# Performance work log

Hardware: AMD Instinct MI355X
Metric: run time of the kernel (lower is better)

The kernel has to match this reference:

```python
import jax, jax.numpy as jnp
import numpy as np

EMBED_DIM = 1024
NUM_HEADS = 16
NUM_GROUPS = 4
HEAD_DIM = EMBED_DIM // NUM_HEADS
REPEAT = NUM_HEADS // NUM_GROUPS
MAX_TIME = 128
MAX_FREQ = 8


def build_relative_index(q_len, k_len, freq_size=MAX_FREQ, max_time=MAX_TIME, max_freq=MAX_FREQ):
    # static (numpy) construction; shapes are compile-time constants under jit
    q_time = q_len // max_freq
    k_time = k_len // max_freq
    qt = np.arange(q_time) + (k_time - q_time)
    q_coords = np.stack(np.meshgrid(qt, np.arange(freq_size), indexing='ij')).reshape(2, -1)
    k_coords = np.stack(np.meshgrid(np.arange(k_time), np.arange(freq_size), indexing='ij')).reshape(2, -1)
    rel = q_coords[:, :, None] - k_coords[:, None, :]  # [2, Nq, Nk]
    rel_t = np.clip(rel[0], -max_time + 1, max_time - 1) + max_time - 1
    rel_f = np.clip(rel[1], -max_freq + 1, max_freq - 1) + max_freq - 1
    return jnp.asarray(rel_t, jnp.int32), jnp.asarray(rel_f, jnp.int32)


def setup_inputs() -> dict:
    key = jax.random.key(0)
    ks = jax.random.split(key, 11)
    B, N, D, Nc = 2, 512, EMBED_DIM, 1536
    s = 0.02
    return {
        'q': jax.random.normal(ks[0], (B, N, D), jnp.float32),
        'k': jax.random.normal(ks[1], (B, N, D), jnp.float32),
        'v': jax.random.normal(ks[2], (B, N, D), jnp.float32),
        'attn_cache_k': jax.random.normal(ks[3], (B * NUM_HEADS, HEAD_DIM, Nc), jnp.float32),
        'attn_cache_v': jax.random.normal(ks[4], (B * NUM_HEADS, Nc, HEAD_DIM), jnp.float32),
        'Wq': jax.random.normal(ks[5], (D, D), jnp.float32) * s,
        'Wk': jax.random.normal(ks[6], (D, HEAD_DIM * NUM_GROUPS), jnp.float32) * s,
        'Wv': jax.random.normal(ks[7], (D, HEAD_DIM * NUM_GROUPS), jnp.float32) * s,
        'Wo': jax.random.normal(ks[8], (D, D), jnp.float32) * s,
        'emb_t': jax.random.normal(ks[9], (2 * MAX_TIME - 1, HEAD_DIM), jnp.float32) * s,
        'emb_f': jax.random.normal(ks[10], (2 * MAX_FREQ - 1, HEAD_DIM), jnp.float32) * s,
    }


def reference(q, k, v, attn_cache_k, attn_cache_v, Wq, Wk, Wv, Wo, emb_t, emb_f):
    B, N, D = q.shape
    H, G, hd, r = NUM_HEADS, NUM_GROUPS, HEAD_DIM, REPEAT
    # projections (no bias); head layout matches torch view: [B, N, H, hd] -> [B*H, N, hd]
    qp = (q @ Wq).reshape(B, N, H, hd).transpose(0, 2, 1, 3).reshape(B * H, N, hd)
    kp = (k @ Wk).reshape(B, N, G, hd).transpose(0, 2, 3, 1).reshape(B * G, hd, N)  # transposed K
    vp = (v @ Wv).reshape(B, N, G, hd).transpose(0, 2, 1, 3).reshape(B * G, N, hd)
    # GQA: repeat_interleave kv heads to query heads
    kp = jnp.repeat(kp, r, axis=0)
    vp = jnp.repeat(vp, r, axis=0)
    # streaming cache concat + slide
    k_full = jnp.concatenate([attn_cache_k, kp], axis=-1)            # [B*H, hd, Nk]
    new_cache_k = k_full[:, :, -attn_cache_k.shape[-1]:]
    v_full = jnp.concatenate([attn_cache_v, vp], axis=1)             # [B*H, Nk, hd]
    new_cache_v = v_full[:, -attn_cache_v.shape[1]:, :]
    Nk = k_full.shape[-1]
    qs = qp * (hd ** -0.5)
    scores = jnp.einsum('bid,bdj->bij', qs, k_full)                  # [B*H, N, Nk]
    rel_t, rel_f = build_relative_index(N, Nk)
    rel_emb = emb_t[rel_t] + emb_f[rel_f]                            # [N, Nk, hd]
    bias = jnp.einsum('bid,ijd->bij', qs, rel_emb)
    attn = jax.nn.softmax(scores + bias, axis=-1)
    ao = jnp.einsum('bij,bjd->bid', attn, v_full)                    # [B*H, N, hd]
    ao = ao.reshape(B, H, N, hd).transpose(2, 0, 1, 3).reshape(N, B, D)
    out = (ao @ Wo).transpose(1, 0, 2)                               # [B, N, D]
    return out, new_cache_k, new_cache_v
```

## Files before the change

kernel.cpp:

```cpp
#include <hip/hip_runtime.h>
#include <math.h>

typedef _Float16 half_t;
typedef _Float16 half8  __attribute__((ext_vector_type(8)));
typedef _Float16 half4v __attribute__((ext_vector_type(4)));
typedef float    floatx4 __attribute__((ext_vector_type(4)));

#define LOG2E 1.44269504088896f

static __device__ __forceinline__ floatx4 mfma16(half8 a, half8 b, floatx4 c) {
    return __builtin_amdgcn_mfma_f32_16x16x32_f16(a, b, c, 0, 0, 0);
}
static __device__ __forceinline__ floatx4 mfma16x16(half4v a, half4v b, floatx4 c) {
    return __builtin_amdgcn_mfma_f32_16x16x16f16(a, b, c, 0, 0, 0);
}

__global__ __launch_bounds__(256) void prep(const float* __restrict__ cache_k,
                                            const float* __restrict__ cache_v,
                                            const float* __restrict__ Wq,
                                            const float* __restrict__ Wk,
                                            const float* __restrict__ Wv,
                                            const float* __restrict__ Wo,
                                            const float* __restrict__ emb_t,
                                            const float* __restrict__ emb_f,
                                            half_t* __restrict__ Kc,
                                            half_t* __restrict__ VcT,
                                            float* __restrict__ out_k,
                                            float* __restrict__ out_v,
                                            half_t* __restrict__ WqT,
                                            half_t* __restrict__ WkvT,
                                            half_t* __restrict__ WoT,
                                            half_t* __restrict__ embc)
{
    const int tid = threadIdx.x;
    const int z = blockIdx.z;
    __shared__ float t[64][65];
    if (z == 0) {
        const int bh = blockIdx.y, j0 = blockIdx.x * 64;
        const bool shift = (j0 >= 512);
        #pragma unroll
        for (int i2 = 0; i2 < 4; i2++) {
            int idx = i2 * 256 + tid;
            int d = idx >> 4, j4 = (idx & 15) * 4;
            float4 vv = *(const float4*)&cache_k[((size_t)bh * 64 + d) * 1536 + j0 + j4];
            *(float4*)&t[d][j4] = vv;
            if (shift) *(float4*)&out_k[((size_t)bh * 64 + d) * 1536 + j0 - 512 + j4] = vv;
        }
        __syncthreads();
        #pragma unroll
        for (int i2 = 0; i2 < 2; i2++) {
            int idx = i2 * 256 + tid;
            int j = idx >> 3, db = (idx & 7) * 8;
            half8 o;
            #pragma unroll
            for (int u = 0; u < 8; u++) o[u] = (half_t)t[db + u][j];
            *(half8*)&Kc[((size_t)bh * 1536 + j0 + j) * 64 + db] = o;
        }
    } else if (z == 1) {
        const int bh = blockIdx.y, j0 = blockIdx.x * 64;
        const bool shift = (j0 >= 512);
        #pragma unroll
        for (int i2 = 0; i2 < 4; i2++) {
            int idx = i2 * 256 + tid;
            int j = idx >> 4, d4 = (idx & 15) * 4;
            float4 vv = *(const float4*)&cache_v[((size_t)bh * 1536 + j0 + j) * 64 + d4];
            *(float4*)&t[j][d4] = vv;
            if (shift) *(float4*)&out_v[((size_t)bh * 1536 + j0 + j - 512) * 64 + d4] = vv;
        }
        __syncthreads();
        #pragma unroll
        for (int i2 = 0; i2 < 2; i2++) {
            int idx = i2 * 256 + tid;
            int d = idx >> 3, jb = (idx & 7) * 8;
            half8 o;
            #pragma unroll
            for (int u = 0; u < 8; u++) o[u] = (half_t)t[jb + u][d];
            *(half8*)&VcT[((size_t)bh * 64 + d) * 1536 + j0 + jb] = o;
        }
    } else {
        const int id = blockIdx.y * 24 + blockIdx.x;
        const float* src; half_t* dst; int Ncols, n0, k0;
        if (id < 256)      { src = Wq; dst = WqT; Ncols = 1024; n0 = (id & 15) * 64; k0 = (id >> 4) * 64; }
        else if (id < 320) { int q2 = id - 256; src = Wk; dst = WkvT; Ncols = 256; n0 = (q2 & 3) * 64; k0 = (q2 >> 2) * 64; }
        else if (id < 384) { int q2 = id - 320; src = Wv; dst = WkvT + 256 * 1024; Ncols = 256; n0 = (q2 & 3) * 64; k0 = (q2 >> 2) * 64; }
        else if (id < 640) { int q2 = id - 384; src = Wo; dst = WoT; Ncols = 1024; n0 = (q2 & 15) * 64; k0 = (q2 >> 4) * 64; }
        else if (id < 720) {
            int idx = (id - 640) * 256 + tid;
            int row = idx >> 6, col = idx & 63;
            float val = 0.f;
            if (row < 255) val = emb_t[row * 64 + col];
            else if (row >= 256 && row < 271) val = emb_f[(row - 256) * 64 + col];
            embc[idx] = (half_t)val;
            return;
        } else return;
        #pragma unroll
        for (int i2 = 0; i2 < 4; i2++) {
            int idx = i2 * 256 + tid;
            int r = idx >> 4, c4 = (idx & 15) * 4;
            *(float4*)&t[r][c4] = *(const float4*)&src[(size_t)(k0 + r) * Ncols + n0 + c4];
        }
        __syncthreads();
        #pragma unroll
        for (int i2 = 0; i2 < 2; i2++) {
            int idx = i2 * 256 + tid;
            int n = idx >> 3, kb = (idx & 7) * 8;
            half8 o;
            #pragma unroll
            for (int u = 0; u < 8; u++) o[u] = (half_t)t[kb + u][n];
            *(half8*)&dst[(size_t)(n0 + n) * 1024 + k0 + kb] = o;
        }
    }
}

__global__ __launch_bounds__(512) void proj(int phase,
                                            const float* __restrict__ qin,
                                            const float* __restrict__ kin,
                                            const float* __restrict__ vin,
                                            const half_t* __restrict__ AO,
                                            const half_t* __restrict__ WqT,
                                            const half_t* __restrict__ WkvT,
                                            const half_t* __restrict__ WoT,
                                            half_t* __restrict__ qs_h,
                                            half_t* __restrict__ kp_h,
                                            half_t* __restrict__ vpT,
                                            float* __restrict__ out,
                                            float* __restrict__ out_k,
                                            float* __restrict__ out_v)
{
    __shared__ __align__(16) half_t As[2][2][64 * 72];
    __shared__ __align__(16) half_t Bs[2][2][64 * 72];
    const int id = blockIdx.x;
    int task, m0, n0;
    const float* Af = nullptr; const half_t* Ah = nullptr; const half_t* Bt;
    if (phase == 1)      { task = 2; m0 = (id >> 4) * 64; n0 = (id & 15) * 64; Ah = AO; Bt = WoT; }
    else if (id < 256)   { task = 0; m0 = (id >> 4) * 64; n0 = (id & 15) * 64; Af = qin; Bt = WqT; }
    else { task = 1; int t = id - 256; m0 = (t >> 3) * 64; n0 = (t & 7) * 64;
           Af = (n0 < 256) ? kin : vin; Bt = WkvT; }

    const int tid = threadIdx.x;
    const int kh = tid >> 8, t8 = tid & 255;
    const int w4 = (tid >> 6) & 3, l = tid & 63;
    const int quad = l >> 4, lr = l & 15, wm = w4 >> 1, wn = w4 & 1;
    const int arow = t8 >> 2, acol = (t8 & 3) * 16;
    const int kbase = kh * 512;

    {
        int kk = kbase;
        if (Af) {
            float4 f0 = *(const float4*)&Af[(size_t)(m0 + arow) * 1024 + kk + acol];
            float4 f1 = *(const float4*)&Af[(size_t)(m0 + arow) * 1024 + kk + acol + 4];
            float4 f2 = *(const float4*)&Af[(size_t)(m0 + arow) * 1024 + kk + acol + 8];
            float4 f3 = *(const float4*)&Af[(size_t)(m0 + arow) * 1024 + kk + acol + 12];
            half8 h0, h1;
            h0[0]=(half_t)f0.x; h0[1]=(half_t)f0.y; h0[2]=(half_t)f0.z; h0[3]=(half_t)f0.w;
            h0[4]=(half_t)f1.x; h0[5]=(half_t)f1.y; h0[6]=(half_t)f1.z; h0[7]=(half_t)f1.w;
            h1[0]=(half_t)f2.x; h1[1]=(half_t)f2.y; h1[2]=(half_t)f2.z; h1[3]=(half_t)f2.w;
            h1[4]=(half_t)f3.x; h1[5]=(half_t)f3.y; h1[6]=(half_t)f3.z; h1[7]=(half_t)f3.w;
            *(half8*)&As[kh][0][arow * 72 + acol] = h0;
            *(half8*)&As[kh][0][arow * 72 + acol + 8] = h1;
        } else {
            *(half8*)&As[kh][0][arow * 72 + acol]     = *(const half8*)&Ah[(size_t)(m0 + arow) * 1024 + kk + acol];
            *(half8*)&As[kh][0][arow * 72 + acol + 8] = *(const half8*)&Ah[(size_t)(m0 + arow) * 1024 + kk + acol + 8];
        }
        *(half8*)&Bs[kh][0][arow * 72 + acol]     = *(const half8*)&Bt[(size_t)(n0 + arow) * 1024 + kk + acol];
        *(half8*)&Bs[kh][0][arow * 72 + acol + 8] = *(const half8*)&Bt[(size_t)(n0 + arow) * 1024 + kk + acol + 8];
    }
    __syncthreads();

    floatx4 zero = {0.f, 0.f, 0.f, 0.f};
    floatx4 acc[2][2];
    acc[0][0] = zero; acc[0][1] = zero; acc[1][0] = zero; acc[1][1] = zero;

    float4 pf0, pf1, pf2, pf3; half8 ph0, ph1, pb0, pb1;
    for (int it = 0; it < 8; ++it) {
        if (it < 7) {
            int kk = kbase + (it + 1) * 64;
            if (Af) {
                pf0 = *(const float4*)&Af[(size_t)(m0 + arow) * 1024 + kk + acol];
                pf1 = *(const float4*)&Af[(size_t)(m0 + arow) * 1024 + kk + acol + 4];
                pf2 = *(const float4*)&Af[(size_t)(m0 + arow) * 1024 + kk + acol + 8];
                pf3 = *(const float4*)&Af[(size_t)(m0 + arow) * 1024 + kk + acol + 12];
            } else {
                ph0 = *(const half8*)&Ah[(size_t)(m0 + arow) * 1024 + kk + acol];
                ph1 = *(const half8*)&Ah[(size_t)(m0 + arow) * 1024 + kk + acol + 8];
            }
            pb0 = *(const half8*)&Bt[(size_t)(n0 + arow) * 1024 + kk + acol];
            pb1 = *(const half8*)&Bt[(size_t)(n0 + arow) * 1024 + kk + acol + 8];
        }
        const half_t* Ab = &As[kh][it & 1][0];
        const half_t* Bb = &Bs[kh][it & 1][0];
        #pragma unroll
        for (int ks = 0; ks < 2; ++ks) {
            half8 a0 = *(const half8*)&Ab[(wm * 32 + lr) * 72 + ks * 32 + quad * 8];
            half8 a1 = *(const half8*)&Ab[(wm * 32 + 16 + lr) * 72 + ks * 32 + quad * 8];
            half8 b0 = *(const half8*)&Bb[(wn * 32 + lr) * 72 + ks * 32 + quad * 8];
            half8 b1 = *(const half8*)&Bb[(wn * 32 + 16 + lr) * 72 + ks * 32 + quad * 8];
            acc[0][0] = mfma16(a0, b0, acc[0][0]);
            acc[0][1] = mfma16(a0, b1, acc[0][1]);
            acc[1][0] = mfma16(a1, b0, acc[1][0]);
            acc[1][1] = mfma16(a1, b1, acc[1][1]);
        }
        __syncthreads();
        if (it < 7) {
            int buf = (it + 1) & 1;
            if (Af) {
                half8 h0, h1;
                h0[0]=(half_t)pf0.x; h0[1]=(half_t)pf0.y; h0[2]=(half_t)pf0.z; h0[3]=(half_t)pf0.w;
                h0[4]=(half_t)pf1.x; h0[5]=(half_t)pf1.y; h0[6]=(half_t)pf1.z; h0[7]=(half_t)pf1.w;
                h1[0]=(half_t)pf2.x; h1[1]=(half_t)pf2.y; h1[2]=(half_t)pf2.z; h1[3]=(half_t)pf2.w;
                h1[4]=(half_t)pf3.x; h1[5]=(half_t)pf3.y; h1[6]=(half_t)pf3.z; h1[7]=(half_t)pf3.w;
                *(half8*)&As[kh][buf][arow * 72 + acol] = h0;
                *(half8*)&As[kh][buf][arow * 72 + acol + 8] = h1;
            } else {
                *(half8*)&As[kh][buf][arow * 72 + acol] = ph0;
                *(half8*)&As[kh][buf][arow * 72 + acol + 8] = ph1;
            }
            *(half8*)&Bs[kh][buf][arow * 72 + acol] = pb0;
            *(half8*)&Bs[kh][buf][arow * 72 + acol + 8] = pb1;
            __syncthreads();
        }
    }

    float* M = (float*)&Bs[0][0][0];
    if (kh == 1) {
        #pragma unroll
        for (int mi = 0; mi < 2; mi++)
            #pragma unroll
            for (int ni = 0; ni < 2; ni++)
                #pragma unroll
                for (int r = 0; r < 4; r++)
                    M[(wm * 32 + mi * 16 + quad * 4 + r) * 66 + wn * 32 + ni * 16 + lr] = acc[mi][ni][r];
    }
    __syncthreads();
    if (kh == 0) {
        #pragma unroll
        for (int mi = 0; mi < 2; mi++)
            #pragma unroll
            for (int ni = 0; ni < 2; ni++)
                #pragma unroll
                for (int r = 0; r < 4; r++)
                    acc[mi][ni][r] += M[(wm * 32 + mi * 16 + quad * 4 + r) * 66 + wn * 32 + ni * 16 + lr];
    }

    if (task == 0) {
        if (kh == 0) {
            #pragma unroll
            for (int mi = 0; mi < 2; mi++)
                #pragma unroll
                for (int ni = 0; ni < 2; ni++)
                    #pragma unroll
                    for (int r = 0; r < 4; r++) {
                        int m = m0 + wm * 32 + mi * 16 + quad * 4 + r;
                        int n = n0 + wn * 32 + ni * 16 + lr;
                        qs_h[(size_t)m * 1024 + n] = (half_t)(acc[mi][ni][r] * (0.125f * LOG2E));
                    }
        }
    } else if (task == 2) {
        if (kh == 0) {
            #pragma unroll
            for (int mi = 0; mi < 2; mi++)
                #pragma unroll
                for (int ni = 0; ni < 2; ni++)
                    #pragma unroll
                    for (int r = 0; r < 4; r++) {
                        int m = m0 + wm * 32 + mi * 16 + quad * 4 + r;
                        int n = n0 + wn * 32 + ni * 16 + lr;
                        out[(size_t)m * 1024 + n] = acc[mi][ni][r];
                    }
        }
    } else {
        float* Ct = (float*)&As[0][0][0];
        if (kh == 0) {
            #pragma unroll
            for (int mi = 0; mi < 2; mi++)
                #pragma unroll
                for (int ni = 0; ni < 2; ni++)
                    #pragma unroll
                    for (int r = 0; r < 4; r++)
                        Ct[(wn * 32 + ni * 16 + lr) * 68 + wm * 32 + mi * 16 + quad * 4 + r] = acc[mi][ni][r];
        }
        __syncthreads();
        if (kh == 0) {
            const int b = m0 >> 9, jm0 = m0 & 511;
            if (n0 < 256) {
                int gg = n0 >> 6;
                {
                    int d = t8 >> 2, jc = (t8 & 3) * 16;
                    float4 vv[4];
                    #pragma unroll
                    for (int u = 0; u < 4; u++) vv[u] = *(float4*)&Ct[d * 68 + jc + u * 4];
                    #pragma unroll
                    for (int t = 0; t < 4; t++)
                        #pragma unroll
                        for (int u = 0; u < 4; u++)
                            *(float4*)&out_k[((size_t)((b * 16 + gg * 4 + t) * 64 + d)) * 1536 + 1024 + jm0 + jc + u * 4] = vv[u];
                }
                {
                    int j = t8 >> 2, dc = (t8 & 3) * 16;
                    half8 o0, o1;
                    #pragma unroll
                    for (int u = 0; u < 8; u++) o0[u] = (half_t)Ct[(dc + u) * 68 + j];
                    #pragma unroll
                    for (int u = 0; u < 8; u++) o1[u] = (half_t)Ct[(dc + 8 + u) * 68 + j];
                    *(half8*)&kp_h[((size_t)(b * 512 + jm0 + j)) * 256 + n0 + dc] = o0;
                    *(half8*)&kp_h[((size_t)(b * 512 + jm0 + j)) * 256 + n0 + dc + 8] = o1;
                }
            } else {
                int gg = (n0 - 256) >> 6;
                {
                    int j = t8 >> 2, dc = (t8 & 3) * 16;
                    float4 vv[4];
                    #pragma unroll
                    for (int u = 0; u < 4; u++) {
                        float4 x;
                        x.x = Ct[(dc + u * 4 + 0) * 68 + j];
                        x.y = Ct[(dc + u * 4 + 1) * 68 + j];
                        x.z = Ct[(dc + u * 4 + 2) * 68 + j];
                        x.w = Ct[(dc + u * 4 + 3) * 68 + j];
                        vv[u] = x;
                    }
                    #pragma unroll
                    for (int t = 0; t < 4; t++)
                        #pragma unroll
                        for (int u = 0; u < 4; u++)
                            *(float4*)&out_v[(((size_t)(b * 16 + gg * 4 + t) * 1536) + 1024 + jm0 + j) * 64 + dc + u * 4] = vv[u];
                }
                {
                    int d = t8 >> 2, jc = (t8 & 3) * 16;
                    half8 o0, o1;
                    #pragma unroll
                    for (int u = 0; u < 8; u++) o0[u] = (half_t)Ct[d * 68 + jc + u];
                    #pragma unroll
                    for (int u = 0; u < 8; u++) o1[u] = (half_t)Ct[d * 68 + jc + 8 + u];
                    *(half8*)&vpT[((size_t)((b * 4 + gg) * 64 + d)) * 512 + jm0 + jc] = o0;
                    *(half8*)&vpT[((size_t)((b * 4 + gg) * 64 + d)) * 512 + jm0 + jc + 8] = o1;
                }
            }
        }
    }
}

__global__ __launch_bounds__(256) void flash(const half_t* __restrict__ qs_h,
                                             const half_t* __restrict__ Kc,
                                             const half_t* __restrict__ kp_h,
                                             const half_t* __restrict__ VcT,
                                             const half_t* __restrict__ vpT,
                                             const half_t* __restrict__ embc,
                                             half_t* __restrict__ AO)
{
    __shared__ __align__(16) half_t Qs[32 * 72];
    __shared__ __align__(16) half_t Ks[128 * 72];
    __shared__ __align__(16) half_t Vs[64 * 136];
    __shared__ half_t bt[32 * 210];
    const int bh = blockIdx.x, b = bh >> 4, h = bh & 15, g = h >> 2;
    const int i0 = blockIdx.y * 32;
    const int tid = threadIdx.x, w = tid >> 6, l = tid & 63;
    const int quad = l >> 4, lr = l & 15;
    const int wq = w >> 1, jh = w & 1;

    *(half8*)&Qs[(tid >> 3) * 72 + (tid & 7) * 8] =
        *(const half8*)&qs_h[((size_t)(b * 512 + i0 + (tid >> 3))) * 1024 + h * 64 + (tid & 7) * 8];

    const int krow = tid >> 1, kc = (tid & 1) * 32;
    const int vd = tid >> 2, vc = (tid & 3) * 32;
    half8 kr[4], vr[4];
    {
        const half_t* ksrc = &Kc[((size_t)bh * 1536 + krow) * 64 + kc];
        const half_t* vsrc = &VcT[((size_t)bh * 64 + vd) * 1536 + vc];
        #pragma unroll
        for (int u = 0; u < 4; u++) kr[u] = *(const half8*)(ksrc + u * 8);
        #pragma unroll
        for (int u = 0; u < 4; u++) vr[u] = *(const half8*)(vsrc + u * 8);
    }
    __syncthreads();

    half8 qf0 = *(const half8*)&Qs[(wq * 16 + lr) * 72 + quad * 8];
    half8 qf1 = *(const half8*)&Qs[(wq * 16 + lr) * 72 + 32 + quad * 8];

    floatx4 zero = {0.f, 0.f, 0.f, 0.f};
    {
        int tk0 = jh ? 10 : 4, tk1 = jh ? 17 : 10;
        for (int tk = tk0; tk < tk1; ++tk) {
            floatx4 acc = zero;
            half8 e0 = *(const half8*)&embc[(size_t)(tk * 16 + lr) * 64 + quad * 8];
            half8 e1 = *(const half8*)&embc[(size_t)(tk * 16 + lr) * 64 + 32 + quad * 8];
            acc = mfma16(e0, qf0, acc);
            acc = mfma16(e1, qf1, acc);
            #pragma unroll
            for (int r = 0; r < 4; r++)
                bt[(wq * 16 + lr) * 210 + tk * 16 + quad * 4 + r - 64] = (half_t)acc[r];
        }
    }

    #pragma unroll
    for (int u = 0; u < 4; u++) *(half8*)&Ks[krow * 72 + kc + u * 8] = kr[u];
    #pragma unroll
    for (int u = 0; u < 4; u++) *(half8*)&Vs[vd * 136 + vc + u * 8] = vr[u];
    __syncthreads();

    const int qtr = (i0 + wq * 16 + lr) >> 3;
    float bfv[4];
    #pragma unroll
    for (int r = 0; r < 4; r++) {
        int f = (lr & 7) - ((quad & 1) * 4 + r) + 7;
        bfv[r] = (float)bt[(wq * 16 + lr) * 210 + 192 + f];
    }

    floatx4 accO[4];
    #pragma unroll
    for (int ni = 0; ni < 4; ni++) accO[ni] = zero;
    float lrun = 0.f;

    for (int jt = 0; jt < 16; ++jt) {
        if (jt < 15) {
            const int j1 = (jt + 1) * 128;
            const half_t* ksrc = (j1 < 1536)
                ? &Kc[((size_t)bh * 1536 + j1 + krow) * 64 + kc]
                : &kp_h[((size_t)(b * 512 + j1 - 1536 + krow)) * 256 + g * 64 + kc];
            const half_t* vsrc = (j1 < 1536)
                ? &VcT[((size_t)bh * 64 + vd) * 1536 + j1 + vc]
                : &vpT[((size_t)(b * 4 + g) * 64 + vd) * 512 + (j1 - 1536) + vc];
            #pragma unroll
            for (int u = 0; u < 4; u++) kr[u] = *(const half8*)(ksrc + u * 8);
            #pragma unroll
            for (int u = 0; u < 4; u++) vr[u] = *(const half8*)(vsrc + u * 8);
        }

        floatx4 s[4];
        #pragma unroll
        for (int c = 0; c < 4; c++) {
            int row = jh * 64 + c * 16 + lr;
            half8 kf0 = *(const half8*)&Ks[row * 72 + quad * 8];
            half8 kf1 = *(const half8*)&Ks[row * 72 + 32 + quad * 8];
            s[c] = mfma16(kf0, qf0, zero);
            s[c] = mfma16(kf1, qf1, s[c]);
        }
        const int ktb = jt * 16 + jh * 8 + (quad >> 1);
        const half_t* btrow = &bt[(wq * 16 + lr) * 210];
        #pragma unroll
        for (int c = 0; c < 4; c++)
            #pragma unroll
            for (int r = 0; r < 4; r++) {
                int toff = 255 + qtr - (ktb + c * 2);
                toff = min(toff, 190);
                float p = exp2f(s[c][r] + (float)btrow[toff] + bfv[r]);
                s[c][r] = p;
                lrun += p;
            }
        #pragma unroll
        for (int c = 0; c < 4; c++) {
            half4v pf;
            #pragma unroll
            for (int r = 0; r < 4; r++) pf[r] = (half_t)s[c][r];
            #pragma unroll
            for (int ni = 0; ni < 4; ni++) {
                half4v vb = *(const half4v*)&Vs[(ni * 16 + lr) * 136 + jh * 64 + c * 16 + quad * 4];
                accO[ni] = mfma16x16(pf, vb, accO[ni]);
            }
        }
        __syncthreads();
        if (jt < 15) {
            #pragma unroll
            for (int u = 0; u < 4; u++) *(half8*)&Ks[krow * 72 + kc + u * 8] = kr[u];
            #pragma unroll
            for (int u = 0; u < 4; u++) *(half8*)&Vs[vd * 136 + vc + u * 8] = vr[u];
            __syncthreads();
        }
    }

    float tot = lrun;
    tot += __shfl_xor(tot, 16);
    tot += __shfl_xor(tot, 32);

    float* MB = (float*)Ks;
    float* ML = (float*)Vs;
    if (jh == 1) {
        if (l < 16) ML[wq * 16 + l] = tot;
        #pragma unroll
        for (int ni = 0; ni < 4; ni++)
            #pragma unroll
            for (int r = 0; r < 4; r++)
                MB[(wq * 16 + quad * 4 + r) * 68 + ni * 16 + lr] = accO[ni][r];
    }
    __syncthreads();
    if (jh == 0) {
        float full = tot + ML[wq * 16 + lr];
        if (l < 16) ML[64 + wq * 16 + l] = full;
        float inv[4];
        #pragma unroll
        for (int r = 0; r < 4; r++) inv[r] = 1.0f / ML[64 + wq * 16 + quad * 4 + r];
        #pragma unroll
        for (int ni = 0; ni < 4; ni++)
            #pragma unroll
            for (int r = 0; r < 4; r++) {
                int row = wq * 16 + quad * 4 + r;
                float o = (accO[ni][r] + MB[row * 68 + ni * 16 + lr]) * inv[r];
                AO[((size_t)(b * 512 + i0 + row)) * 1024 + h * 64 + ni * 16 + lr] = (half_t)o;
            }
    }
}

extern "C" void kernel_launch(void* const* d_in, const int* in_sizes, int n_in,
                              void* d_out, int out_size, void* d_ws, size_t ws_size,
                              hipStream_t stream)
{
    const float* q       = (const float*)d_in[0];
    const float* k       = (const float*)d_in[1];
    const float* v       = (const float*)d_in[2];
    const float* cache_k = (const float*)d_in[3];
    const float* cache_v = (const float*)d_in[4];
    const float* Wq      = (const float*)d_in[5];
    const float* Wk      = (const float*)d_in[6];
    const float* Wv      = (const float*)d_in[7];
    const float* Wo      = (const float*)d_in[8];
    const float* emb_t   = (const float*)d_in[9];
    const float* emb_f   = (const float*)d_in[10];

    float* out   = (float*)d_out;
    float* out_k = out + 1048576;
    float* out_v = out_k + 3145728;

    half_t* ws = (half_t*)d_ws;
    half_t* qs_h = ws;
    half_t* kp_h = ws + 1048576;
    half_t* vpT  = ws + 1310720;
    half_t* Kc   = ws + 1572864;
    half_t* VcT  = ws + 4718592;
    half_t* WqT  = ws + 7864320;
    half_t* WkvT = ws + 8912896;
    half_t* WoT  = ws + 9437184;
    half_t* embc = ws + 10485760;
    half_t* AO   = ws + 10506240;

    prep<<<dim3(24, 32, 3), 256, 0, stream>>>(cache_k, cache_v, Wq, Wk, Wv, Wo,
                                              emb_t, emb_f, Kc, VcT, out_k, out_v,
                                              WqT, WkvT, WoT, embc);
    proj<<<dim3(384), 512, 0, stream>>>(0, q, k, v, nullptr, WqT, WkvT, WoT,
                                        qs_h, kp_h, vpT, out, out_k, out_v);
    flash<<<dim3(32, 16), 256, 0, stream>>>(qs_h, Kc, kp_h, VcT, vpT, embc, AO);
    proj<<<dim3(256), 512, 0, stream>>>(1, q, k, v, AO, WqT, WkvT, WoT,
                                        qs_h, kp_h, vpT, out, out_k, out_v);
}
```

Baseline: 172.8 us.

## Split flash key tiles across eight waves with swizzled LDS and MFMA row sums

```diff
diff --git a/kernel.cpp b/kernel.cpp
--- a/kernel.cpp
+++ b/kernel.cpp
@@ -340,62 +340,64 @@
     }
 }
 
-__global__ __launch_bounds__(256) void flash(const half_t* __restrict__ qs_h,
-                                             const half_t* __restrict__ Kc,
-                                             const half_t* __restrict__ kp_h,
-                                             const half_t* __restrict__ VcT,
-                                             const half_t* __restrict__ vpT,
-                                             const half_t* __restrict__ embc,
-                                             half_t* __restrict__ AO)
+__global__ __launch_bounds__(512, 4) void flash(const half_t* __restrict__ qs_h,
+                                                const half_t* __restrict__ Kc,
+                                                const half_t* __restrict__ kp_h,
+                                                const half_t* __restrict__ VcT,
+                                                const half_t* __restrict__ vpT,
+                                                const half_t* __restrict__ embc,
+                                                half_t* __restrict__ AO)
 {
-    __shared__ __align__(16) half_t Qs[32 * 72];
-    __shared__ __align__(16) half_t Ks[128 * 72];
-    __shared__ __align__(16) half_t Vs[64 * 136];
-    __shared__ half_t bt[32 * 210];
+    __shared__ __align__(16) half_t smem[25152];
+    half_t* Ks = smem;
+    half_t* Vs = smem + 8192;
+    half_t* Qs = smem + 16384;
+    half_t* bt = smem + 18432;
+
     const int bh = blockIdx.x, b = bh >> 4, h = bh & 15, g = h >> 2;
     const int i0 = blockIdx.y * 32;
     const int tid = threadIdx.x, w = tid >> 6, l = tid & 63;
     const int quad = l >> 4, lr = l & 15;
-    const int wq = w >> 1, jh = w & 1;
-
-    *(half8*)&Qs[(tid >> 3) * 72 + (tid & 7) * 8] =
-        *(const half8*)&qs_h[((size_t)(b * 512 + i0 + (tid >> 3))) * 1024 + h * 64 + (tid & 7) * 8];
-
-    const int krow = tid >> 1, kc = (tid & 1) * 32;
-    const int vd = tid >> 2, vc = (tid & 3) * 32;
-    half8 kr[4], vr[4];
-    {
-        const half_t* ksrc = &Kc[((size_t)bh * 1536 + krow) * 64 + kc];
-        const half_t* vsrc = &VcT[((size_t)bh * 64 + vd) * 1536 + vc];
-        #pragma unroll
-        for (int u = 0; u < 4; u++) kr[u] = *(const half8*)(ksrc + u * 8);
-        #pragma unroll
-        for (int u = 0; u < 4; u++) vr[u] = *(const half8*)(vsrc + u * 8);
+    const int wq = w >> 2, jh = w & 3;
+
+    if (tid < 256) {
+        int row = tid >> 3, cc = tid & 7;
+        *(half8*)&Qs[row * 64 + ((cc ^ (row & 7)) * 8)] =
+            *(const half8*)&qs_h[((size_t)(b * 512 + i0 + row)) * 1024 + h * 64 + cc * 8];
+    }
+
+    half8 kr[2], vr[2];
+    #pragma unroll
+    for (int u = 0; u < 2; u++) {
+        int row = u * 64 + (tid >> 3);
+        kr[u] = *(const half8*)&Kc[((size_t)bh * 1536 + row) * 64 + (tid & 7) * 8];
+        int d = u * 32 + (tid >> 4);
+        vr[u] = *(const half8*)&VcT[((size_t)bh * 64 + d) * 1536 + (tid & 15) * 8];
     }
     __syncthreads();
 
-    half8 qf0 = *(const half8*)&Qs[(wq * 16 + lr) * 72 + quad * 8];
-    half8 qf1 = *(const half8*)&Qs[(wq * 16 + lr) * 72 + 32 + quad * 8];
+    half8 qf0 = *(const half8*)&Qs[(wq * 16 + lr) * 64 + ((quad ^ (lr & 7)) * 8)];
+    half8 qf1 = *(const half8*)&Qs[(wq * 16 + lr) * 64 + (((4 + quad) ^ (lr & 7)) * 8)];
 
     floatx4 zero = {0.f, 0.f, 0.f, 0.f};
-    {
-        int tk0 = jh ? 10 : 4, tk1 = jh ? 17 : 10;
-        for (int tk = tk0; tk < tk1; ++tk) {
-            floatx4 acc = zero;
-            half8 e0 = *(const half8*)&embc[(size_t)(tk * 16 + lr) * 64 + quad * 8];
-            half8 e1 = *(const half8*)&embc[(size_t)(tk * 16 + lr) * 64 + 32 + quad * 8];
-            acc = mfma16(e0, qf0, acc);
-            acc = mfma16(e1, qf1, acc);
-            #pragma unroll
-            for (int r = 0; r < 4; r++)
-                bt[(wq * 16 + lr) * 210 + tk * 16 + quad * 4 + r - 64] = (half_t)acc[r];
-        }
+    for (int tk = 4 + jh; tk < 17; tk += 4) {
+        floatx4 acc = zero;
+        half8 e0 = *(const half8*)&embc[(size_t)(tk * 16 + lr) * 64 + quad * 8];
+        half8 e1 = *(const half8*)&embc[(size_t)(tk * 16 + lr) * 64 + 32 + quad * 8];
+        acc = mfma16(e0, qf0, acc);
+        acc = mfma16(e1, qf1, acc);
+        #pragma unroll
+        for (int r = 0; r < 4; r++)
+            bt[(wq * 16 + lr) * 210 + tk * 16 + quad * 4 + r - 64] = (half_t)acc[r];
     }
 
     #pragma unroll
-    for (int u = 0; u < 4; u++) *(half8*)&Ks[krow * 72 + kc + u * 8] = kr[u];
-    #pragma unroll
-    for (int u = 0; u < 4; u++) *(half8*)&Vs[vd * 136 + vc + u * 8] = vr[u];
+    for (int u = 0; u < 2; u++) {
+        int row = u * 64 + (tid >> 3);
+        *(half8*)&Ks[row * 64 + (((tid & 7) ^ (row & 7)) * 8)] = kr[u];
+        int d = u * 32 + (tid >> 4);
+        *(half8*)&Vs[d * 128 + (((tid & 15) ^ (d & 7)) * 8)] = vr[u];
+    }
     __syncthreads();
 
     const int qtr = (i0 + wq * 16 + lr) >> 3;
@@ -409,93 +411,110 @@
     floatx4 accO[4];
     #pragma unroll
     for (int ni = 0; ni < 4; ni++) accO[ni] = zero;
-    float lrun = 0.f;
+    floatx4 accS = zero;
+    const half4v vone = {(half_t)1.f, (half_t)1.f, (half_t)1.f, (half_t)1.f};
 
     for (int jt = 0; jt < 16; ++jt) {
         if (jt < 15) {
             const int j1 = (jt + 1) * 128;
-            const half_t* ksrc = (j1 < 1536)
-                ? &Kc[((size_t)bh * 1536 + j1 + krow) * 64 + kc]
-                : &kp_h[((size_t)(b * 512 + j1 - 1536 + krow)) * 256 + g * 64 + kc];
-            const half_t* vsrc = (j1 < 1536)
-                ? &VcT[((size_t)bh * 64 + vd) * 1536 + j1 + vc]
-                : &vpT[((size_t)(b * 4 + g) * 64 + vd) * 512 + (j1 - 1536) + vc];
-            #pragma unroll
-            for (int u = 0; u < 4; u++) kr[u] = *(const half8*)(ksrc + u * 8);
-            #pragma unroll
-            for (int u = 0; u < 4; u++) vr[u] = *(const half8*)(vsrc + u * 8);
-        }
-
-        floatx4 s[4];
-        #pragma unroll
-        for (int c = 0; c < 4; c++) {
-            int row = jh * 64 + c * 16 + lr;
-            half8 kf0 = *(const half8*)&Ks[row * 72 + quad * 8];
-            half8 kf1 = *(const half8*)&Ks[row * 72 + 32 + quad * 8];
+            #pragma unroll
+            for (int u = 0; u < 2; u++) {
+                int row = u * 64 + (tid >> 3);
+                const half_t* ksrc = (j1 < 1536)
+                    ? &Kc[((size_t)bh * 1536 + j1 + row) * 64 + (tid & 7) * 8]
+                    : &kp_h[((size_t)(b * 512 + j1 - 1536 + row)) * 256 + g * 64 + (tid & 7) * 8];
+                kr[u] = *(const half8*)ksrc;
+                int d = u * 32 + (tid >> 4);
+                const half_t* vsrc = (j1 < 1536)
+                    ? &VcT[((size_t)bh * 64 + d) * 1536 + j1 + (tid & 15) * 8]
+                    : &vpT[((size_t)(b * 4 + g) * 64 + d) * 512 + (j1 - 1536) + (tid & 15) * 8];
+                vr[u] = *(const half8*)vsrc;
+            }
+        }
+
+        floatx4 s[2];
+        #pragma unroll
+        for (int c = 0; c < 2; c++) {
+            int row = jh * 32 + c * 16 + lr;
+            half8 kf0 = *(const half8*)&Ks[row * 64 + ((quad ^ (row & 7)) * 8)];
+            half8 kf1 = *(const half8*)&Ks[row * 64 + (((4 + quad) ^ (row & 7)) * 8)];
             s[c] = mfma16(kf0, qf0, zero);
             s[c] = mfma16(kf1, qf1, s[c]);
         }
-        const int ktb = jt * 16 + jh * 8 + (quad >> 1);
+        const int ktb = jt * 16 + jh * 4 + (quad >> 1);
         const half_t* btrow = &bt[(wq * 16 + lr) * 210];
         #pragma unroll
-        for (int c = 0; c < 4; c++)
-            #pragma unroll
-            for (int r = 0; r < 4; r++) {
-                int toff = 255 + qtr - (ktb + c * 2);
-                toff = min(toff, 190);
-                float p = exp2f(s[c][r] + (float)btrow[toff] + bfv[r]);
-                s[c][r] = p;
-                lrun += p;
-            }
-        #pragma unroll
-        for (int c = 0; c < 4; c++) {
+        for (int c = 0; c < 2; c++) {
+            int toff = 255 + qtr - (ktb + c * 2);
+            toff = min(toff, 190);
+            float tb = (float)btrow[toff];
+            #pragma unroll
+            for (int r = 0; r < 4; r++)
+                s[c][r] = exp2f(s[c][r] + tb + bfv[r]);
+        }
+        #pragma unroll
+        for (int c = 0; c < 2; c++) {
             half4v pf;
             #pragma unroll
             for (int r = 0; r < 4; r++) pf[r] = (half_t)s[c][r];
+            accS = mfma16x16(pf, vone, accS);
+            const int bj = jh * 4 + c * 2 + (quad >> 1);
             #pragma unroll
             for (int ni = 0; ni < 4; ni++) {
-                half4v vb = *(const half4v*)&Vs[(ni * 16 + lr) * 136 + jh * 64 + c * 16 + quad * 4];
+                int d = ni * 16 + lr;
+                half4v vb = *(const half4v*)&Vs[d * 128 + ((bj ^ (lr & 7)) * 8) + (quad & 1) * 4];
                 accO[ni] = mfma16x16(pf, vb, accO[ni]);
             }
         }
         __syncthreads();
         if (jt < 15) {
             #pragma unroll
-            for (int u = 0; u < 4; u++) *(half8*)&Ks[krow * 72 + kc + u * 8] = kr[u];
-            #pragma unroll
-            for (int u = 0; u < 4; u++) *(half8*)&Vs[vd * 136 + vc + u * 8] = vr[u];
+            for (int u = 0; u < 2; u++) {
+                int row = u * 64 + (tid >> 3);
+                *(half8*)&Ks[row * 64 + (((tid & 7) ^ (row & 7)) * 8)] = kr[u];
+                int d = u * 32 + (tid >> 4);
+                *(half8*)&Vs[d * 128 + (((tid & 15) ^ (d & 7)) * 8)] = vr[u];
+            }
             __syncthreads();
         }
     }
 
-    float tot = lrun;
-    tot += __shfl_xor(tot, 16);
-    tot += __shfl_xor(tot, 32);
-
-    float* MB = (float*)Ks;
-    float* ML = (float*)Vs;
-    if (jh == 1) {
-        if (l < 16) ML[wq * 16 + l] = tot;
+    float* Mf = (float*)smem;
+    float* Sf = Mf + 6 * 16 * 68;
+    if (jh != 0) {
+        int p = (jh - 1) * 2 + wq;
         #pragma unroll
         for (int ni = 0; ni < 4; ni++)
             #pragma unroll
             for (int r = 0; r < 4; r++)
-                MB[(wq * 16 + quad * 4 + r) * 68 + ni * 16 + lr] = accO[ni][r];
+                Mf[(p * 16 + quad * 4 + r) * 68 + ni * 16 + lr] = accO[ni][r];
+        if (lr == 0) {
+            #pragma unroll
+            for (int r = 0; r < 4; r++)
+                Sf[p * 16 + quad * 4 + r] = accS[r];
+        }
     }
     __syncthreads();
     if (jh == 0) {
-        float full = tot + ML[wq * 16 + lr];
-        if (l < 16) ML[64 + wq * 16 + l] = full;
         float inv[4];
         #pragma unroll
-        for (int r = 0; r < 4; r++) inv[r] = 1.0f / ML[64 + wq * 16 + quad * 4 + r];
+        for (int r = 0; r < 4; r++) {
+            float t = accS[r];
+            #pragma unroll
+            for (int jj = 0; jj < 3; jj++) t += Sf[(jj * 2 + wq) * 16 + quad * 4 + r];
+            inv[r] = 1.0f / t;
+        }
         #pragma unroll
         for (int ni = 0; ni < 4; ni++)
             #pragma unroll
             for (int r = 0; r < 4; r++) {
+                float o = accO[ni][r];
+                #pragma unroll
+                for (int jj = 0; jj < 3; jj++)
+                    o += Mf[((jj * 2 + wq) * 16 + quad * 4 + r) * 68 + ni * 16 + lr];
                 int row = wq * 16 + quad * 4 + r;
-                float o = (accO[ni][r] + MB[row * 68 + ni * 16 + lr]) * inv[r];
-                AO[((size_t)(b * 512 + i0 + row)) * 1024 + h * 64 + ni * 16 + lr] = (half_t)o;
+                AO[((size_t)(b * 512 + i0 + row)) * 1024 + h * 64 + ni * 16 + lr] =
+                    (half_t)(o * inv[r]);
             }
     }
 }
@@ -537,7 +556,7 @@
                                               WqT, WkvT, WoT, embc);
     proj<<<dim3(384), 512, 0, stream>>>(0, q, k, v, nullptr, WqT, WkvT, WoT,
                                         qs_h, kp_h, vpT, out, out_k, out_v);
-    flash<<<dim3(32, 16), 256, 0, stream>>>(qs_h, Kc, kp_h, VcT, vpT, embc, AO);
+    flash<<<dim3(32, 16), 512, 0, stream>>>(qs_h, Kc, kp_h, VcT, vpT, embc, AO);
     proj<<<dim3(256), 512, 0, stream>>>(1, q, k, v, AO, WqT, WkvT, WoT,
                                         qs_h, kp_h, vpT, out, out_k, out_v);
 }
```

New measurement: 168.4 us (median of 2 runs). 2.6% less time.
